# Kernel tuning notes

Measured on AMD Instinct MI355X. Metric: run time of the kernel, lower is better.

The kernel has to match this reference:

```python
import jax, jax.numpy as jnp
import numpy as np

B, S, D, H = 2, 2048, 1024, 16
HS = D // H  # head_size = 64


def setup_inputs() -> dict:
    key = jax.random.key(0)
    k1, k2, k3 = jax.random.split(key, 3)
    x = jax.random.normal(k1, (B, S, D), dtype=jnp.float32)
    c_attn_w = jax.random.normal(k2, (D, 3 * D), dtype=jnp.float32) * (1.0 / np.sqrt(D))
    c_attn_b = jnp.zeros((3 * D,), dtype=jnp.float32)
    c_proj_w = jax.random.normal(k3, (D, D), dtype=jnp.float32) * (1.0 / np.sqrt(D))
    c_proj_b = jnp.zeros((D,), dtype=jnp.float32)
    return {"x": x, "c_attn_w": c_attn_w, "c_attn_b": c_attn_b,
            "c_proj_w": c_proj_w, "c_proj_b": c_proj_b}


def reference(x, c_attn_w, c_attn_b, c_proj_w, c_proj_b):
    b, s, d = x.shape
    qkv = x @ c_attn_w + c_attn_b  # [b, s, 3d]
    q, k, v = jnp.split(qkv, 3, axis=-1)
    # [b, h, s, hs]
    q = q.reshape(b, s, H, HS).transpose(0, 2, 1, 3)
    k = k.reshape(b, s, H, HS).transpose(0, 2, 1, 3)
    v = v.reshape(b, s, H, HS).transpose(0, 2, 1, 3)
    scale = jnp.float32(HS) ** -0.5
    scores = jnp.einsum('bhqd,bhkd->bhqk', q, k) * scale  # [b, h, s, s]
    causal = jnp.tril(jnp.ones((s, s), dtype=bool))
    scores = jnp.where(causal[None, None, :, :], scores, jnp.float32(-jnp.inf))
    weights = jax.nn.softmax(scores, axis=-1)  # attn_dropout p=0 -> identity
    attn = jnp.einsum('bhqk,bhkd->bhqd', weights, v)  # [b, h, s, hs]
    attn = attn.transpose(0, 2, 1, 3).reshape(b, s, d)
    out = attn @ c_proj_w + c_proj_b  # resid_dropout p=0 -> identity
    return out
```

## Files before the change

### kernel.cpp

```cpp
#include <hip/hip_runtime.h>
#include <hip/hip_bf16.h>
#include <stdint.h>

#define TB 2
#define TS 2048
#define TD 1024
#define TH 16
#define THS 64
#define TK 1024

typedef __attribute__((ext_vector_type(8))) short short8;
typedef __attribute__((ext_vector_type(4))) short short4v;
typedef __attribute__((ext_vector_type(4))) float f32x4;
typedef __attribute__((ext_vector_type(16))) float f32x16;
typedef __attribute__((ext_vector_type(4))) unsigned int uint4v;

static __device__ __forceinline__ unsigned short f2bf(float f) {
  union { float f; unsigned u; } v; v.f = f;
  unsigned r = v.u + 0x7FFFu + ((v.u >> 16) & 1u);
  return (unsigned short)(r >> 16);
}

static __device__ __forceinline__ unsigned cvtpk(float a, float b) {
  unsigned r;
  asm("v_cvt_pk_bf16_f32 %0, %1, %2" : "=v"(r) : "v"(a), "v"(b));
  return r;
}

static __device__ __forceinline__ void swap32(unsigned& a, unsigned& b) {
  asm("v_permlane32_swap_b32 %0, %1" : "+v"(a), "+v"(b));
}

static __device__ __forceinline__ void async_copy16(const void* g, void* l) {
  __builtin_amdgcn_global_load_lds(
      (const __attribute__((address_space(1))) unsigned int*)g,
      (__attribute__((address_space(3))) unsigned int*)l, 16, 0, 0);
}

__global__ __launch_bounds__(256) void k_cvt_bf16x4(const float* __restrict__ in,
                                                    ushort4* __restrict__ out, int n4) {
  int i = blockIdx.x * blockDim.x + threadIdx.x;
  if (i >= n4) return;
  float4 v = ((const float4*)in)[i];
  out[i] = make_ushort4(f2bf(v.x), f2bf(v.y), f2bf(v.z), f2bf(v.w));
}

__global__ __launch_bounds__(256) void k_transpose_bf(const float* __restrict__ in,
                                                      unsigned short* __restrict__ out,
                                                      int R, int C) {
  __shared__ float tile[32][33];
  const int tx = threadIdx.x & 31, ty = threadIdx.x >> 5;
  const int r0 = blockIdx.y * 32, c0 = blockIdx.x * 32;
#pragma unroll
  for (int i = 0; i < 32; i += 8)
    tile[ty + i][tx] = in[(size_t)(r0 + ty + i) * C + c0 + tx];
  __syncthreads();
#pragma unroll
  for (int i = 0; i < 32; i += 8)
    out[(size_t)(c0 + ty + i) * R + r0 + tx] = f2bf(tile[tx][ty + i]);
}

__device__ __forceinline__ void gemm_core_k1024(const unsigned short* __restrict__ A,
                                                const unsigned short* __restrict__ BT,
                                                int m0, int n0,
                                                unsigned short* sA, unsigned short* sB,
                                                f32x4 acc[4][4]) {
  const int tid = threadIdx.x;
  const int wave = tid >> 6, lane = tid & 63;
  const int wm = wave >> 1, wn = wave & 1;

  const unsigned short* gsrc = (wave < 2) ? A : BT;
  const int row0 = (wave < 2) ? m0 : n0;
  unsigned short* lbase = (wave < 2) ? sA : sB;
  const int cw = (wave & 1) * 4;
  const size_t gr = (size_t)(row0 + cw * 16 + (lane >> 2)) * TK + (lane & 3) * 8;

#pragma unroll
  for (int mi = 0; mi < 4; ++mi)
#pragma unroll
    for (int ni = 0; ni < 4; ++ni)
      acc[mi][ni] = (f32x4){0.f, 0.f, 0.f, 0.f};

  auto stage = [&](int buf, int kt) {
    const unsigned short* g = gsrc + gr + kt * 32;
    unsigned short* l = lbase + buf * 4096 + cw * 512;
#pragma unroll
    for (int c = 0; c < 4; ++c)
      async_copy16(g + (size_t)c * 16 * TK, l + c * 512);
  };

  stage(0, 0);
  __syncthreads();

  const int l15 = lane & 15, lk8 = (lane >> 4) * 8;
  const int aoff = (wm * 64 + l15) * 32 + lk8;
  const int boff = (wn * 64 + l15) * 32 + lk8;

  for (int kt = 0; kt < TK / 32; ++kt) {
    const int buf = kt & 1;
    if (kt + 1 < TK / 32) stage(buf ^ 1, kt + 1);
    short8 af[4], bfr[4];
#pragma unroll
    for (int i = 0; i < 4; ++i) {
      af[i] = *(const short8*)&sA[buf * 4096 + aoff + i * 16 * 32];
      bfr[i] = *(const short8*)&sB[buf * 4096 + boff + i * 16 * 32];
    }
#pragma unroll
    for (int mi = 0; mi < 4; ++mi)
#pragma unroll
      for (int ni = 0; ni < 4; ++ni)
        acc[mi][ni] = __builtin_amdgcn_mfma_f32_16x16x32_bf16(af[mi], bfr[ni], acc[mi][ni], 0, 0, 0);
    __syncthreads();
  }
}

__global__ __launch_bounds__(256) void k_gemm_qkv(const unsigned short* __restrict__ A,
                                                  const unsigned short* __restrict__ BT,
                                                  const float* __restrict__ bias,
                                                  unsigned short* __restrict__ Qo,
                                                  unsigned short* __restrict__ Ko,
                                                  unsigned short* __restrict__ VTo) {
  __shared__ unsigned short smem[4 * 64 * 68];
  unsigned short* sA = smem;
  unsigned short* sB = smem + 8192;
  f32x4 acc[4][4];
  const int m0 = blockIdx.y * 128, n0 = blockIdx.x * 128;
  gemm_core_k1024(A, BT, m0, n0, sA, sB, acc);

  const int lane = threadIdx.x & 63, wave = threadIdx.x >> 6;
  const int wm = wave >> 1, wn = wave & 1;
  const int lr4 = (lane >> 4) * 4, l15 = lane & 15;

  const int col0 = n0 + wn * 64;
  const int reg = col0 >> 10;
  const int h0 = (col0 & 1023) >> 6;
  const bool isV = (reg == 2);
  const int t0 = m0 + wm * 64;
  const int b = t0 >> 11;
  const int s0 = t0 & 2047;

  unsigned short* tw = smem + wave * (64 * 68);
#pragma unroll
  for (int mi = 0; mi < 4; ++mi) {
#pragma unroll
    for (int ni = 0; ni < 4; ++ni) {
      const int c = ni * 16 + l15;
      const float bi = bias[col0 + c];
#pragma unroll
      for (int j = 0; j < 4; ++j) {
        const int r = mi * 16 + lr4 + j;
        tw[isV ? (c * 68 + r) : (r * 68 + c)] = f2bf(acc[mi][ni][j] + bi);
      }
    }
  }
  unsigned short* outp;
  size_t rstride;
  if (isV) {
    outp = VTo + (((size_t)b * TH + h0) * THS) * TS + s0;
    rstride = TS;
  } else {
    outp = (reg == 0 ? Qo : Ko) + (((size_t)b * TH + h0) * TS + s0) * THS;
    rstride = THS;
  }
#pragma unroll
  for (int p2 = 0; p2 < 8; ++p2) {
    const int rp = p2 * 8 + (lane >> 3);
    const int co = (lane & 7) * 8;
    union { short4v h[2]; short8 s8; } u;
    u.h[0] = *(const short4v*)&tw[rp * 68 + co];
    u.h[1] = *(const short4v*)&tw[rp * 68 + co + 4];
    *(short8*)(outp + (size_t)rp * rstride + co) = u.s8;
  }
}

__global__ __launch_bounds__(256) void k_attn(const unsigned short* __restrict__ Q,
                                              const unsigned short* __restrict__ K,
                                              const unsigned short* __restrict__ VT,
                                              unsigned short* __restrict__ attn) {
  __shared__ unsigned short sO[4][32 * 68];
  const int lane = threadIdx.x & 63, wave = threadIdx.x >> 6;
  const int l31 = lane & 31, h = lane >> 5;
  int qt = blockIdx.x;
  const int hh = blockIdx.y, b = blockIdx.z;
  if (b) qt = 15 - qt;
  const int qrb = qt * 128 + wave * 32;

  const unsigned short* Qh = Q + (((size_t)b * TH + hh) * TS) * THS;
  const unsigned short* Kh = K + (((size_t)b * TH + hh) * TS) * THS;
  const unsigned short* Vh = VT + (((size_t)b * TH + hh) * THS) * TS;

  short8 qf[4];
#pragma unroll
  for (int c2 = 0; c2 < 4; ++c2)
    qf[c2] = *(const short8*)&Qh[(size_t)(qrb + l31) * THS + c2 * 16 + h * 8];

  f32x16 o0 = {}, o1 = {};
  float m_run = -1e30f, l_run = 0.f;
  const float cl2e = 0.125f * 1.44269504088896340736f;

  const int nkt = (qrb >> 5) + 1;

  short8 kf[4];
#pragma unroll
  for (int c2 = 0; c2 < 4; ++c2)
    kf[c2] = *(const short8*)&Kh[(size_t)l31 * THS + c2 * 16 + h * 8];

  for (int kt = 0; kt < nkt; ++kt) {
    const int kb = kt * 32;
    short8 vf[2][2];
#pragma unroll
    for (int t = 0; t < 2; ++t)
#pragma unroll
      for (int c2 = 0; c2 < 2; ++c2)
        vf[t][c2] = *(const short8*)&Vh[(size_t)(t * 32 + l31) * TS + kb + c2 * 16 + h * 8];

    f32x16 s = {};
#pragma unroll
    for (int c2 = 0; c2 < 4; ++c2)
      s = __builtin_amdgcn_mfma_f32_32x32x16_bf16(kf[c2], qf[c2], s, 0, 0, 0);

    if (kt + 1 < nkt) {
#pragma unroll
      for (int c2 = 0; c2 < 4; ++c2)
        kf[c2] = *(const short8*)&Kh[(size_t)(kb + 32 + l31) * THS + c2 * 16 + h * 8];
    }

    if (kt == nkt - 1) {
#pragma unroll
      for (int r = 0; r < 16; ++r)
        if ((r & 3) + 8 * (r >> 2) + 4 * h > l31) s[r] = -1e30f;
    }

    float tm = s[0];
#pragma unroll
    for (int r = 1; r < 16; ++r) tm = fmaxf(tm, s[r]);
    tm = fmaxf(tm, __shfl_xor(tm, 32));
    const float mn = fmaxf(m_run, tm);
    const float al = __builtin_amdgcn_exp2f((m_run - mn) * cl2e);
    m_run = mn;
    float ts = 0.f;
#pragma unroll
    for (int r = 0; r < 16; ++r) {
      const float p = __builtin_amdgcn_exp2f((s[r] - mn) * cl2e);
      s[r] = p;
      ts += p;
    }
    ts += __shfl_xor(ts, 32);
    l_run = l_run * al + ts;
    o0 *= al;
    o1 *= al;

    unsigned B0 = cvtpk(s[0], s[1]), B1 = cvtpk(s[2], s[3]);
    unsigned B2 = cvtpk(s[4], s[5]), B3 = cvtpk(s[6], s[7]);
    swap32(B0, B2);
    swap32(B1, B3);
    unsigned B4 = cvtpk(s[8], s[9]), B5 = cvtpk(s[10], s[11]);
    unsigned B6 = cvtpk(s[12], s[13]), B7 = cvtpk(s[14], s[15]);
    swap32(B4, B6);
    swap32(B5, B7);
    union U { uint4v u; short8 s8; } u0, u1;
    u0.u = (uint4v){B0, B1, B2, B3};
    u1.u = (uint4v){B4, B5, B6, B7};

    o0 = __builtin_amdgcn_mfma_f32_32x32x16_bf16(vf[0][0], u0.s8, o0, 0, 0, 0);
    o0 = __builtin_amdgcn_mfma_f32_32x32x16_bf16(vf[0][1], u1.s8, o0, 0, 0, 0);
    o1 = __builtin_amdgcn_mfma_f32_32x32x16_bf16(vf[1][0], u0.s8, o1, 0, 0, 0);
    o1 = __builtin_amdgcn_mfma_f32_32x32x16_bf16(vf[1][1], u1.s8, o1, 0, 0, 0);
  }

  const float inv = 1.0f / l_run;
  unsigned* so32 = (unsigned*)&sO[wave][0];
#pragma unroll
  for (int j2 = 0; j2 < 8; ++j2) {
    const int d0 = ((2 * j2) & 3) + 8 * (j2 >> 1) + 4 * h;
    so32[l31 * 34 + (d0 >> 1)] = cvtpk(o0[2 * j2] * inv, o0[2 * j2 + 1] * inv);
    so32[l31 * 34 + ((32 + d0) >> 1)] = cvtpk(o1[2 * j2] * inv, o1[2 * j2 + 1] * inv);
  }
#pragma unroll
  for (int p2 = 0; p2 < 4; ++p2) {
    const int rp = p2 * 8 + (lane >> 3);
    const int co = (lane & 7) * 8;
    short4v va = *(const short4v*)&sO[wave][rp * 68 + co];
    short4v vb = *(const short4v*)&sO[wave][rp * 68 + co + 4];
    unsigned short* gp = &attn[(size_t)(b * TS + qrb + rp) * TD + hh * THS + co];
    *(short4v*)gp = va;
    *(short4v*)(gp + 4) = vb;
  }
}

__global__ __launch_bounds__(256) void k_gemm_proj(const unsigned short* __restrict__ A,
                                                   const unsigned short* __restrict__ BT,
                                                   const float* __restrict__ bias,
                                                   float* __restrict__ out) {
  __shared__ unsigned short sA[2 * 4096];
  __shared__ unsigned short sB[2 * 4096];
  f32x4 acc[4][4];
  const int m0 = blockIdx.y * 128, n0 = blockIdx.x * 128;
  gemm_core_k1024(A, BT, m0, n0, sA, sB, acc);

  const int lane = threadIdx.x & 63, wave = threadIdx.x >> 6;
  const int wm = wave >> 1, wn = wave & 1;
  const int lr4 = (lane >> 4) * 4, l15 = lane & 15;
#pragma unroll
  for (int mi = 0; mi < 4; ++mi) {
    const int row = m0 + wm * 64 + mi * 16 + lr4;
#pragma unroll
    for (int ni = 0; ni < 4; ++ni) {
      const int col = n0 + wn * 64 + ni * 16 + l15;
      const float bi = bias[col];
#pragma unroll
      for (int j = 0; j < 4; ++j)
        out[(size_t)(row + j) * TD + col] = acc[mi][ni][j] + bi;
    }
  }
}

extern "C" void kernel_launch(void* const* d_in, const int* in_sizes, int n_in,
                              void* d_out, int out_size, void* d_ws, size_t ws_size,
                              hipStream_t stream) {
  const float* x = (const float*)d_in[0];
  const float* c_attn_w = (const float*)d_in[1];
  const float* c_attn_b = (const float*)d_in[2];
  const float* c_proj_w = (const float*)d_in[3];
  const float* c_proj_b = (const float*)d_in[4];
  float* out = (float*)d_out;

  const size_t SZ_XB = (size_t)4096 * 1024 * 2;
  const size_t SZ_WAT = (size_t)3072 * 1024 * 2;
  const size_t SZ_WPT = (size_t)1024 * 1024 * 2;
  const size_t SZ_HEAD = (size_t)TB * TH * TS * THS * 2;
  const size_t SZ_ATT = (size_t)4096 * 1024 * 2;
  if (ws_size < SZ_XB + SZ_WAT + SZ_WPT + 3 * SZ_HEAD + SZ_ATT) return;

  char* ws = (char*)d_ws;
  unsigned short* xb = (unsigned short*)ws;   ws += SZ_XB;
  unsigned short* waT = (unsigned short*)ws;  ws += SZ_WAT;
  unsigned short* wpT = (unsigned short*)ws;  ws += SZ_WPT;
  unsigned short* Qb = (unsigned short*)ws;   ws += SZ_HEAD;
  unsigned short* Kb = (unsigned short*)ws;   ws += SZ_HEAD;
  unsigned short* VTb = (unsigned short*)ws;  ws += SZ_HEAD;
  unsigned short* attn = (unsigned short*)ws; ws += SZ_ATT;

  k_cvt_bf16x4<<<4096, 256, 0, stream>>>(x, (ushort4*)xb, 4096 * 1024 / 4);
  k_transpose_bf<<<dim3(3072 / 32, 1024 / 32), 256, 0, stream>>>(c_attn_w, waT, 1024, 3072);
  k_transpose_bf<<<dim3(1024 / 32, 1024 / 32), 256, 0, stream>>>(c_proj_w, wpT, 1024, 1024);
  k_gemm_qkv<<<dim3(3072 / 128, 4096 / 128), 256, 0, stream>>>(xb, waT, c_attn_b, Qb, Kb, VTb);
  k_attn<<<dim3(16, TH, TB), 256, 0, stream>>>(Qb, Kb, VTb, attn);
  k_gemm_proj<<<dim3(1024 / 128, 4096 / 128), 256, 0, stream>>>(attn, wpT, c_proj_b, out);
}
```

Baseline: 209.2 us.

## Split long causal attention rows across two waves and add combine kernel

Query tiles in the second half of the sequence now split their key range into two halves, each handled by a separate wave. The waves write partial outputs and (max, sum) pairs into reused workspace, and a new combine kernel merges them. This evens out the causal workload across waves and raises parallelism. The change also skips the online-softmax rescale whenever the running max grows by less than a threshold, trading a little numeric headroom for fewer multiplies. The costs are an extra kernel launch and a bf16 round-trip for the partial outputs.

Result: slower. 246.6 us (+17.9%).

```diff
diff --git a/kernel.cpp b/kernel.cpp
--- a/kernel.cpp
+++ b/kernel.cpp
@@ -19,6 +19,11 @@
   union { float f; unsigned u; } v; v.f = f;
   unsigned r = v.u + 0x7FFFu + ((v.u >> 16) & 1u);
   return (unsigned short)(r >> 16);
+}
+
+static __device__ __forceinline__ float bf2f(unsigned short u) {
+  union { unsigned u; float f; } v; v.u = ((unsigned)u) << 16;
+  return v.f;
 }
 
 static __device__ __forceinline__ unsigned cvtpk(float a, float b) {
@@ -176,14 +181,22 @@
 __global__ __launch_bounds__(256) void k_attn(const unsigned short* __restrict__ Q,
                                               const unsigned short* __restrict__ K,
                                               const unsigned short* __restrict__ VT,
-                                              unsigned short* __restrict__ attn) {
+                                              unsigned short* __restrict__ attn,
+                                              unsigned short* __restrict__ pO,
+                                              float2* __restrict__ pML) {
   __shared__ unsigned short sO[4][32 * 68];
   const int lane = threadIdx.x & 63, wave = threadIdx.x >> 6;
   const int l31 = lane & 31, h = lane >> 5;
-  int qt = blockIdx.x;
+  int c = blockIdx.x * 4 + wave;
   const int hh = blockIdx.y, b = blockIdx.z;
-  if (b) qt = 15 - qt;
-  const int qrb = qt * 128 + wave * 32;
+  if (b) c = 95 - c;
+
+  int w, lo, hi, jhalf;
+  if (c < 64) { w = c; lo = 0; hi = (w < 32) ? (w + 1) : 32; jhalf = 0; }
+  else        { w = c - 32; lo = 32; hi = w + 1; jhalf = 1; }
+  const bool partial = (w >= 32);
+  const bool diag = (hi - 1 == w);
+  const int qrb = w * 32;
 
   const unsigned short* Qh = Q + (((size_t)b * TH + hh) * TS) * THS;
   const unsigned short* Kh = K + (((size_t)b * TH + hh) * TS) * THS;
@@ -197,15 +210,14 @@
   f32x16 o0 = {}, o1 = {};
   float m_run = -1e30f, l_run = 0.f;
   const float cl2e = 0.125f * 1.44269504088896340736f;
-
-  const int nkt = (qrb >> 5) + 1;
+  const float THR = 8.0f / cl2e;
 
   short8 kf[4];
 #pragma unroll
   for (int c2 = 0; c2 < 4; ++c2)
-    kf[c2] = *(const short8*)&Kh[(size_t)l31 * THS + c2 * 16 + h * 8];
-
-  for (int kt = 0; kt < nkt; ++kt) {
+    kf[c2] = *(const short8*)&Kh[(size_t)(lo * 32 + l31) * THS + c2 * 16 + h * 8];
+
+  for (int kt = lo; kt < hi; ++kt) {
     const int kb = kt * 32;
     short8 vf[2][2];
 #pragma unroll
@@ -219,36 +231,45 @@
     for (int c2 = 0; c2 < 4; ++c2)
       s = __builtin_amdgcn_mfma_f32_32x32x16_bf16(kf[c2], qf[c2], s, 0, 0, 0);
 
-    if (kt + 1 < nkt) {
+    if (kt + 1 < hi) {
 #pragma unroll
       for (int c2 = 0; c2 < 4; ++c2)
         kf[c2] = *(const short8*)&Kh[(size_t)(kb + 32 + l31) * THS + c2 * 16 + h * 8];
     }
 
-    if (kt == nkt - 1) {
+    if (diag && kt == hi - 1) {
 #pragma unroll
       for (int r = 0; r < 16; ++r)
         if ((r & 3) + 8 * (r >> 2) + 4 * h > l31) s[r] = -1e30f;
     }
 
-    float tm = s[0];
-#pragma unroll
-    for (int r = 1; r < 16; ++r) tm = fmaxf(tm, s[r]);
+    const float ma = fmaxf(fmaxf(s[0], s[1]), fmaxf(s[2], s[3]));
+    const float mb = fmaxf(fmaxf(s[4], s[5]), fmaxf(s[6], s[7]));
+    const float mc = fmaxf(fmaxf(s[8], s[9]), fmaxf(s[10], s[11]));
+    const float md = fmaxf(fmaxf(s[12], s[13]), fmaxf(s[14], s[15]));
+    float tm = fmaxf(fmaxf(ma, mb), fmaxf(mc, md));
     tm = fmaxf(tm, __shfl_xor(tm, 32));
-    const float mn = fmaxf(m_run, tm);
-    const float al = __builtin_amdgcn_exp2f((m_run - mn) * cl2e);
-    m_run = mn;
-    float ts = 0.f;
-#pragma unroll
-    for (int r = 0; r < 16; ++r) {
-      const float p = __builtin_amdgcn_exp2f((s[r] - mn) * cl2e);
-      s[r] = p;
-      ts += p;
-    }
+
+    float al;
+    if (__all(tm <= m_run + THR)) {
+      al = 1.0f;
+    } else {
+      const float mn = fmaxf(m_run, tm);
+      al = __builtin_amdgcn_exp2f((m_run - mn) * cl2e);
+      m_run = mn;
+      o0 *= al;
+      o1 *= al;
+    }
+#pragma unroll
+    for (int r = 0; r < 16; ++r)
+      s[r] = __builtin_amdgcn_exp2f((s[r] - m_run) * cl2e);
+    const float sa = (s[0] + s[1]) + (s[2] + s[3]);
+    const float sb2 = (s[4] + s[5]) + (s[6] + s[7]);
+    const float sc = (s[8] + s[9]) + (s[10] + s[11]);
+    const float sd = (s[12] + s[13]) + (s[14] + s[15]);
+    float ts = (sa + sb2) + (sc + sd);
     ts += __shfl_xor(ts, 32);
     l_run = l_run * al + ts;
-    o0 *= al;
-    o1 *= al;
 
     unsigned B0 = cvtpk(s[0], s[1]), B1 = cvtpk(s[2], s[3]);
     unsigned B2 = cvtpk(s[4], s[5]), B3 = cvtpk(s[6], s[7]);
@@ -268,7 +289,7 @@
     o1 = __builtin_amdgcn_mfma_f32_32x32x16_bf16(vf[1][1], u1.s8, o1, 0, 0, 0);
   }
 
-  const float inv = 1.0f / l_run;
+  const float inv = partial ? 1.0f : (1.0f / l_run);
   unsigned* so32 = (unsigned*)&sO[wave][0];
 #pragma unroll
   for (int j2 = 0; j2 < 8; ++j2) {
@@ -276,15 +297,53 @@
     so32[l31 * 34 + (d0 >> 1)] = cvtpk(o0[2 * j2] * inv, o0[2 * j2 + 1] * inv);
     so32[l31 * 34 + ((32 + d0) >> 1)] = cvtpk(o1[2 * j2] * inv, o1[2 * j2 + 1] * inv);
   }
-#pragma unroll
-  for (int p2 = 0; p2 < 4; ++p2) {
-    const int rp = p2 * 8 + (lane >> 3);
-    const int co = (lane & 7) * 8;
-    short4v va = *(const short4v*)&sO[wave][rp * 68 + co];
-    short4v vb = *(const short4v*)&sO[wave][rp * 68 + co + 4];
-    unsigned short* gp = &attn[(size_t)(b * TS + qrb + rp) * TD + hh * THS + co];
-    *(short4v*)gp = va;
-    *(short4v*)(gp + 4) = vb;
+  if (!partial) {
+#pragma unroll
+    for (int p2 = 0; p2 < 4; ++p2) {
+      const int rp = p2 * 8 + (lane >> 3);
+      const int co = (lane & 7) * 8;
+      short4v va = *(const short4v*)&sO[wave][rp * 68 + co];
+      short4v vb = *(const short4v*)&sO[wave][rp * 68 + co + 4];
+      unsigned short* gp = &attn[(size_t)(b * TS + qrb + rp) * TD + hh * THS + co];
+      *(short4v*)gp = va;
+      *(short4v*)(gp + 4) = vb;
+    }
+  } else {
+    const int p = ((b * TH + hh) * 32 + (w - 32)) * 2 + jhalf;
+    unsigned short* gp0 = pO + (size_t)p * 32 * 64;
+#pragma unroll
+    for (int p2 = 0; p2 < 4; ++p2) {
+      const int rp = p2 * 8 + (lane >> 3);
+      const int co = (lane & 7) * 8;
+      union { short4v h[2]; short8 s8; } u;
+      u.h[0] = *(const short4v*)&sO[wave][rp * 68 + co];
+      u.h[1] = *(const short4v*)&sO[wave][rp * 68 + co + 4];
+      *(short8*)(gp0 + rp * 64 + co) = u.s8;
+    }
+    if (h == 0) pML[p * 32 + l31] = make_float2(m_run, l_run);
+  }
+}
+
+__global__ __launch_bounds__(64) void k_attn_combine(const unsigned short* __restrict__ pO,
+                                                     const float2* __restrict__ pML,
+                                                     unsigned short* __restrict__ attn) {
+  const int d = threadIdx.x;
+  const int wx = blockIdx.x;
+  const int hh = blockIdx.y, b = blockIdx.z;
+  const int p = ((b * TH + hh) * 32 + wx) * 2;
+  const float cl2e = 0.125f * 1.44269504088896340736f;
+  const unsigned short* oa = pO + (size_t)p * 32 * 64;
+  const unsigned short* ob = oa + 32 * 64;
+#pragma unroll 4
+  for (int r = 0; r < 32; ++r) {
+    const float2 A = pML[p * 32 + r];
+    const float2 Bv = pML[(p + 1) * 32 + r];
+    const float m = fmaxf(A.x, Bv.x);
+    const float eA = __builtin_amdgcn_exp2f((A.x - m) * cl2e);
+    const float eB = __builtin_amdgcn_exp2f((Bv.x - m) * cl2e);
+    const float linv = 1.0f / (A.y * eA + Bv.y * eB);
+    const float o = (bf2f(oa[r * 64 + d]) * eA + bf2f(ob[r * 64 + d]) * eB) * linv;
+    attn[(size_t)(b * TS + (32 + wx) * 32 + r) * TD + hh * THS + d] = f2bf(o);
   }
 }
 
@@ -341,10 +400,14 @@
   unsigned short* VTb = (unsigned short*)ws;  ws += SZ_HEAD;
   unsigned short* attn = (unsigned short*)ws; ws += SZ_ATT;
 
+  unsigned short* pO = xb;
+  float2* pML = (float2*)waT;
+
   k_cvt_bf16x4<<<4096, 256, 0, stream>>>(x, (ushort4*)xb, 4096 * 1024 / 4);
   k_transpose_bf<<<dim3(3072 / 32, 1024 / 32), 256, 0, stream>>>(c_attn_w, waT, 1024, 3072);
   k_transpose_bf<<<dim3(1024 / 32, 1024 / 32), 256, 0, stream>>>(c_proj_w, wpT, 1024, 1024);
   k_gemm_qkv<<<dim3(3072 / 128, 4096 / 128), 256, 0, stream>>>(xb, waT, c_attn_b, Qb, Kb, VTb);
-  k_attn<<<dim3(16, TH, TB), 256, 0, stream>>>(Qb, Kb, VTb, attn);
+  k_attn<<<dim3(24, TH, TB), 256, 0, stream>>>(Qb, Kb, VTb, attn, pO, pML);
+  k_attn_combine<<<dim3(32, TH, TB), 64, 0, stream>>>(pO, pML, attn);
   k_gemm_proj<<<dim3(1024 / 128, 4096 / 128), 256, 0, stream>>>(attn, wpT, c_proj_b, out);
 }
```
